# Kernel tuning notes

Hardware: AMD Instinct MI355X
Metric: run time of the kernel (lower is better)

Reference implementation:

```python
import jax, jax.numpy as jnp
import numpy as np

B, N, K_H, K_EC = 32, 2048, 50, 5  # graphs, nodes/graph, homophily-knn k, edgeconv k


def _leaky(v):
    return jnp.where(v >= 0, v, 0.01 * v)


def _pairwise_sq(xg):
    # xg: [B,N,F] -> squared euclidean distances [B,N,N]
    s = jnp.sum(xg * xg, axis=-1)
    return s[:, :, None] + s[:, None, :] - 2.0 * jnp.einsum('bnf,bmf->bnm', xg, xg)


def _gather(xg, idx):
    # xg [B,N,F], idx [B,N,k] -> [B,N,k,F]
    return jax.vmap(lambda xs, ix: xs[ix])(xg, idx)


def _edge_conv(xg, w1, b1, w2, b2):
    # DynamicEdgeConv: knn (self included, as PyG knn), msg = nn([x_i, x_j - x_i]), aggr='add'
    d = _pairwise_sq(xg)
    _, idx = jax.lax.top_k(-d, K_EC)          # [B,N,k]
    xj = _gather(xg, idx)                      # [B,N,k,F]
    xi = jnp.broadcast_to(xg[:, :, None, :], xj.shape)
    m = jnp.concatenate([xi, xj - xi], axis=-1)
    h = _leaky(m @ w1 + b1)
    h = _leaky(h @ w2 + b2)
    return h.sum(axis=2)                       # add aggregation -> [B,N,out]


def _homophily(y, idx):
    # y [B,N], idx [B,N,k]: fraction of edges whose endpoints have equal value, per graph
    yj = jax.vmap(lambda ys, ix: ys[ix])(y, idx)
    same = (yj == y[:, :, None]).astype(jnp.float32)
    return same.mean(axis=(1, 2))              # [B]


def reference(x, pos, batch, c1w1, c1b1, c1w2, c1b2, c2w1, c2b1, c2w2, c2b2,
              l1w1, l1b1, l1w2, l1b2, mw1, mb1, mw2, mb2):
    xx = jnp.concatenate([x, pos], axis=1).reshape(B, N, 4)
    # homophily kNN graph (k=50, self-loops excluded as in knn_graph)
    d = _pairwise_sq(xx) + jnp.eye(N, dtype=xx.dtype) * 1e9
    _, hidx = jax.lax.top_k(-d, K_H)
    h = [_homophily(xx[..., c], hidx) for c in range(4)]  # hx,hy,hz,hq each [B]
    x1 = _edge_conv(xx, c1w1, c1b1, c1w2, c1b2)   # [B,N,64]
    x2 = _edge_conv(x1, c2w1, c2b1, c2w2, c2b2)   # shared conv2 weights
    x3 = _edge_conv(x2, c2w1, c2b1, c2w2, c2b2)
    feat = jnp.concatenate([xx, x1, x2, x3], axis=-1)  # [B,N,196]
    o = _leaky(feat @ l1w1 + l1b1) @ l1w2 + l1b2       # lin1 -> [B,N,256]
    o = o.mean(axis=1)                                  # global_mean_pool -> [B,256]
    o = jnp.concatenate([o] + [hh[:, None] for hh in h], axis=1)  # [B,260]
    o = _leaky(o)
    o = _leaky(o @ mw1 + mb1)
    return o @ mw2 + mb2                                # [B,cla]


def setup_inputs() -> dict:
    key = jax.random.key(0)
    ks = jax.random.split(key, 20)

    def lin(k, fin, fout):
        kw, kb = jax.random.split(k)
        s = 1.0 / np.sqrt(fin)
        return (jax.random.uniform(kw, (fin, fout), jnp.float32, -s, s),
                jax.random.uniform(kb, (fout,), jnp.float32, -s, s))

    x = jax.random.normal(ks[0], (B * N, 1), jnp.float32)
    pos = jax.random.normal(ks[1], (B * N, 3), jnp.float32)
    batch = jnp.repeat(jnp.arange(B, dtype=jnp.int64), N)
    c1w1, c1b1 = lin(ks[2], 8, 64)
    c1w2, c1b2 = lin(ks[3], 64, 64)
    c2w1, c2b1 = lin(ks[4], 128, 128)
    c2w2, c2b2 = lin(ks[5], 128, 64)
    l1w1, l1b1 = lin(ks[6], 196, 512)
    l1w2, l1b2 = lin(ks[7], 512, 256)
    mw1, mb1 = lin(ks[8], 260, 256)
    mw2, mb2 = lin(ks[9], 256, 3)
    return dict(x=x, pos=pos, batch=batch,
                c1w1=c1w1, c1b1=c1b1, c1w2=c1w2, c1b2=c1b2,
                c2w1=c2w1, c2b1=c2b1, c2w2=c2w2, c2b2=c2b2,
                l1w1=l1w1, l1b1=l1b1, l1w2=l1w2, l1b2=l1b2,
                mw1=mw1, mb1=mb1, mw2=mw2, mb2=mb2)
```

## Files before the change

### kernel.cpp

```cpp
#include <hip/hip_runtime.h>

static constexpr int B = 32, N = 2048, BN = B * N;

#define DEV static __device__ __forceinline__

typedef _Float16 half_t;
typedef __attribute__((ext_vector_type(8))) _Float16 half8;
typedef __attribute__((ext_vector_type(4))) _Float16 half4;
typedef __attribute__((ext_vector_type(4))) float f32x4;
typedef unsigned long long u64;

DEV float lk(float v) { return v >= 0.f ? v : 0.01f * v; }
DEV bool lexlt(float d1, int j1, float d2, int j2) {
    return d1 < d2 || (d1 == d2 && j1 < j2);
}

DEV unsigned int mono(float f) {
    unsigned int b = __float_as_uint(f);
    return b ^ ((unsigned int)((int)b >> 31) | 0x80000000u);
}
DEV float unmono(unsigned int v) {
    unsigned int b = (v & 0x80000000u) ? (v & 0x7fffffffu) : ~v;
    return __uint_as_float(b);
}
DEV u64 pk(float d, int j) {
    return ((u64)mono(d) << 32) | (unsigned int)j;
}
static constexpr u64 KINIT = 0xFF800000ull << 32 | 0x7fffffffull;

DEV int mbcnt64(unsigned long long m) {
    return __builtin_amdgcn_mbcnt_hi((unsigned)(m >> 32),
                                     __builtin_amdgcn_mbcnt_lo((unsigned)m, 0));
}
DEV float dist4s(float4 a, float sa, float4 b, float sb) {
    float dt = fmaf(a.x, b.x, fmaf(a.y, b.y, fmaf(a.z, b.z, a.w * b.w)));
    return (sa + sb) - 2.f * dt;
}

__global__ __launch_bounds__(256) void k_build_xx(const float* __restrict__ x,
                                                  const float* __restrict__ pos,
                                                  float* __restrict__ xx,
                                                  float* __restrict__ sq) {
    int i = blockIdx.x * 256 + threadIdx.x;
    if (i < BN) {
        float4 v;
        v.x = x[i];
        v.y = pos[3 * i + 0];
        v.z = pos[3 * i + 1];
        v.w = pos[3 * i + 2];
        ((float4*)xx)[i] = v;
        sq[i] = fmaf(v.x, v.x, fmaf(v.y, v.y, fmaf(v.z, v.z, v.w * v.w)));
    }
}

__global__ __launch_bounds__(256, 8) void k_knn4(const float* __restrict__ xx,
                                                 const float* __restrict__ sq,
                                                 int* __restrict__ c1idx,
                                                 unsigned int* __restrict__ hpart) {
    int gw = (blockIdx.x * 256 + threadIdx.x) >> 6;
    int lane = threadIdx.x & 63;
    int g = gw >> 11, i = gw & 2047;
    int lane_self = i & 63, t_self = i >> 6;
    const float4* base = ((const float4*)xx) + g * N;
    const float* sqb = sq + g * N;
    float4 xi = base[i];
    float si = sqb[i];

    unsigned int u[32];
    unsigned int L[6];
    unsigned int eqany = 0;
#pragma unroll
    for (int s = 0; s < 6; s++) L[s] = 0xFFFFFFFFu;
#pragma unroll 4
    for (int t = 0; t < 32; t++) {
        float4 xj = base[lane + 64 * t];
        float sj = sqb[lane + 64 * t];
        unsigned int nv = mono(dist4s(xi, si, xj, sj));
        u[t] = nv;
        bool eq = (xj.x == xi.x) | (xj.y == xi.y) | (xj.z == xi.z) | (xj.w == xi.w);
        bool notself = (lane + 64 * t) != i;
        eqany |= (eq && notself) ? (1u << t) : 0u;
#pragma unroll
        for (int s = 0; s < 6; s++) {
            unsigned int lo_ = min(L[s], nv);
            nv = max(L[s], nv);
            L[s] = lo_;
        }
    }
    unsigned int uself = 0x80000000u;
    bool haveEq = (__ballot(eqany != 0) != 0ULL);

    unsigned int lo = L[0], hi = L[0];
#pragma unroll
    for (int o = 1; o < 64; o <<= 1) {
        lo = min(lo, (unsigned int)__shfl_xor((int)lo, o));
        hi = max(hi, (unsigned int)__shfl_xor((int)hi, o));
    }
    unsigned int cp = lo ^ hi;
    int msb = cp ? (31 - __builtin_clz(cp)) : -1;
    unsigned int prefix = (msb >= 0) ? (hi & ~((2u << msb) - 1u)) : lo;

    unsigned int vA = prefix, vB = prefix;
    if (haveEq) {
#pragma unroll 1
        for (int bit = msb; bit >= 0; --bit) {
            unsigned int cA = vA | (1u << bit);
            unsigned int cB = vB | (1u << bit);
            int cntA = 0, cntB = 0;
#pragma unroll
            for (int s = 0; s < 6; s++) cntA += (int)__popcll(__ballot(L[s] < cA));
#pragma unroll
            for (int s = 0; s < 5; s++) cntB += (int)__popcll(__ballot(L[s] < cB));
            cntA -= (uself < cA) ? 1 : 0;
            if (cntA < 50) vA = cA;
            if (cntB < 5) vB = cB;
        }
        if (__ballot(L[5] < vA) != 0ULL) {
            vA = prefix;
#pragma unroll 1
            for (int bit = msb; bit >= 0; --bit) {
                unsigned int c = vA | (1u << bit);
                int cnt = 0;
#pragma unroll
                for (int t = 0; t < 32; t++) cnt += (int)__popcll(__ballot(u[t] < c));
                cnt -= (uself < c) ? 1 : 0;
                if (cnt < 50) vA = c;
            }
        }
    } else {
#pragma unroll 1
        for (int bit = msb; bit >= 0; --bit) {
            unsigned int cB = vB | (1u << bit);
            int cntB = 0;
#pragma unroll
            for (int s = 0; s < 5; s++) cntB += (int)__popcll(__ballot(L[s] < cB));
            if (cntB < 5) vB = cB;
        }
    }

    unsigned int rawB = 0, eqBm = 0;
#pragma unroll
    for (int t = 0; t < 32; t++) {
        rawB |= (u[t] < vB ? 1u : 0u) << t;
        eqBm |= (u[t] == vB ? 1u : 0u) << t;
    }
    unsigned int packB = (unsigned)__popc(rawB) | ((unsigned)__popc(eqBm) << 16);

    if (haveEq) {
        unsigned int rawA = 0, eqAm = 0;
#pragma unroll
        for (int t = 0; t < 32; t++) {
            rawA |= (u[t] < vA ? 1u : 0u) << t;
            eqAm |= (u[t] == vA ? 1u : 0u) << t;
        }
        unsigned int packA = (unsigned)__popc(rawA) | ((unsigned)__popc(eqAm) << 16);
#pragma unroll
        for (int o = 1; o < 64; o <<= 1) packA += __shfl_xor(packA, o);
        int cltA = (int)(packA & 0xffffu) - ((uself < vA) ? 1 : 0);
        int ceqA = (int)(packA >> 16) - ((uself == vA) ? 1 : 0);

        int neededA = 50 - cltA;
        bool allEqA = (ceqA == neededA);
        unsigned int selAm = rawA, eqAs = eqAm;
        if (lane == lane_self) {
            selAm &= ~(1u << t_self);
            eqAs &= ~(1u << t_self);
        }
        unsigned int hm = allEqA ? (selAm | eqAs) : selAm;
        int c0 = 0, c1 = 0, c2 = 0, c3 = 0;
        unsigned int mm = hm;
        while (mm) {
            int t = __ffs(mm) - 1;
            mm &= mm - 1;
            float4 xj = base[lane + 64 * t];
            c0 += (xj.x == xi.x) ? 1 : 0;
            c1 += (xj.y == xi.y) ? 1 : 0;
            c2 += (xj.z == xi.z) ? 1 : 0;
            c3 += (xj.w == xi.w) ? 1 : 0;
        }
        if (!allEqA) {
            unsigned int em = eqAs;
            for (int r = 0; r < neededA; r++) {
                int mt = __ffs(em) - 1;
                int mj = (mt >= 0) ? (lane + 64 * mt) : 0x7fffffff;
                int bm = mj;
#pragma unroll
                for (int o = 1; o < 64; o <<= 1) bm = min(bm, __shfl_xor(bm, o));
                if (mj == bm && mt >= 0) {
                    em &= ~(1u << mt);
                    float4 xj = base[lane + 64 * mt];
                    c0 += (xj.x == xi.x) ? 1 : 0;
                    c1 += (xj.y == xi.y) ? 1 : 0;
                    c2 += (xj.z == xi.z) ? 1 : 0;
                    c3 += (xj.w == xi.w) ? 1 : 0;
                }
            }
        }
        unsigned int pc = (unsigned)c0 | ((unsigned)c1 << 8) | ((unsigned)c2 << 16) | ((unsigned)c3 << 24);
#pragma unroll
        for (int o = 1; o < 64; o <<= 1) pc += __shfl_xor(pc, o);
        if (lane == 0) hpart[gw] = pc;
    } else {
        if (lane == 0) hpart[gw] = 0u;
    }

#pragma unroll
    for (int o = 1; o < 64; o <<= 1) packB += __shfl_xor(packB, o);
    int cltB = (int)(packB & 0xffffu);
    int ceqB = (int)(packB >> 16);
    int neededB = 5 - cltB;
    bool allEqB = (ceqB == neededB);
    unsigned int selBm = allEqB ? (rawB | eqBm) : rawB;
    int base_slot = 0;
#pragma unroll 4
    for (int t = 0; t < 32; t++) {
        bool take = (selBm >> t) & 1;
        unsigned long long m = __ballot(take);
        if (take) c1idx[gw * 5 + base_slot + mbcnt64(m)] = lane + 64 * t;
        base_slot += (int)__popcll(m);
    }
    if (!allEqB) {
        unsigned int em = eqBm;
        for (int r = 0; r < neededB; r++) {
            int mt = __ffs(em) - 1;
            int mj = (mt >= 0) ? (lane + 64 * mt) : 0x7fffffff;
            int bm = mj;
#pragma unroll
            for (int o = 1; o < 64; o <<= 1) bm = min(bm, __shfl_xor(bm, o));
            if (mj == bm && mt >= 0) {
                em &= ~(1u << mt);
                c1idx[gw * 5 + base_slot + r] = bm;
            }
        }
    }
}

__global__ __launch_bounds__(256) void k_split(const float* __restrict__ X,
                                               half_t* __restrict__ Xh,
                                               half_t* __restrict__ Xl,
                                               float* __restrict__ s) {
    int row = (blockIdx.x * 256 + threadIdx.x) >> 6;
    int lane = threadIdx.x & 63;
    float x = X[(size_t)row * 64 + lane];
    half_t h = (half_t)x;
    half_t l = (half_t)(x - (float)h);
    Xh[(size_t)row * 64 + lane] = h;
    Xl[(size_t)row * 64 + lane] = l;
    float ss = x * x;
#pragma unroll
    for (int o = 1; o < 64; o <<= 1) ss += __shfl_xor(ss, o);
    if (lane == 0) s[row] = ss;
}

template <int F, int C>
__global__ __launch_bounds__(256, 4) void k_pq(const float* __restrict__ X,
                                               const float* __restrict__ w1,
                                               const float* __restrict__ b1,
                                               float* __restrict__ p,
                                               float* __restrict__ q) {
    constexpr int FS = F + 4;
    __shared__ __align__(16) float Xs[64 * FS];
    __shared__ __align__(16) float Ws[64 * FS];
    int nbase = blockIdx.x * 64;
    int cchunk = blockIdx.y;
    int tx = threadIdx.x & 15, ty = threadIdx.x >> 4;
    for (int idx = threadIdx.x; idx < 64 * (F / 4); idx += 256) {
        int r = idx / (F / 4), fq = idx % (F / 4);
        float4 v = ((const float4*)(X + (size_t)(nbase + r) * F))[fq];
        *(float4*)&Xs[r * FS + fq * 4] = v;
    }
    for (int idx = threadIdx.x; idx < 64 * F; idx += 256) {
        int f = idx >> 6, cl = idx & 63;
        int ccg = cchunk * 64 + cl;
        float v;
        if (ccg < C) v = w1[f * C + ccg] - w1[(F + f) * C + ccg];
        else         v = w1[(F + f) * C + (ccg - C)];
        Ws[cl * FS + f] = v;
    }
    __syncthreads();
    float acc[4][4];
#pragma unroll
    for (int a = 0; a < 4; a++)
#pragma unroll
        for (int b = 0; b < 4; b++) acc[a][b] = 0.f;
#pragma unroll 2
    for (int fs = 0; fs < F / 4; fs++) {
        float4 xv[4], wv[4];
#pragma unroll
        for (int a = 0; a < 4; a++) xv[a] = *(const float4*)&Xs[(ty + 16 * a) * FS + fs * 4];
#pragma unroll
        for (int b = 0; b < 4; b++) wv[b] = *(const float4*)&Ws[(tx + 16 * b) * FS + fs * 4];
#pragma unroll
        for (int a = 0; a < 4; a++)
#pragma unroll
            for (int b = 0; b < 4; b++) {
                acc[a][b] = fmaf(xv[a].x, wv[b].x, acc[a][b]);
                acc[a][b] = fmaf(xv[a].y, wv[b].y, acc[a][b]);
                acc[a][b] = fmaf(xv[a].z, wv[b].z, acc[a][b]);
                acc[a][b] = fmaf(xv[a].w, wv[b].w, acc[a][b]);
            }
    }
#pragma unroll
    for (int a = 0; a < 4; a++) {
        int n = nbase + ty + 16 * a;
#pragma unroll
        for (int b = 0; b < 4; b++) {
            int ccg = cchunk * 64 + tx + 16 * b;
            if (ccg < C) p[(size_t)n * C + ccg] = acc[a][b] + b1[ccg];
            else         q[(size_t)n * C + (ccg - C)] = acc[a][b];
        }
    }
}

template <int C1>
__global__ __launch_bounds__(256, 4) void k_edge(const float* __restrict__ p,
                                                 const float* __restrict__ q,
                                                 const int* __restrict__ cidx,
                                                 const float* __restrict__ w2,
                                                 const float* __restrict__ b2,
                                                 float* __restrict__ Xout) {
    __shared__ __align__(16) float h1[80 * 68];
    __shared__ __align__(16) float w2T[64 * 68];
    int nb = blockIdx.x * 16;
    int gb = (nb >> 11) << 11;
    int tx = threadIdx.x & 15, ty = threadIdx.x >> 4;
    float acc[5][4];
#pragma unroll
    for (int m = 0; m < 5; m++)
#pragma unroll
        for (int n = 0; n < 4; n++) acc[m][n] = 0.f;
#pragma unroll 1
    for (int half = 0; half < C1 / 64; half++) {
        __syncthreads();
        for (int idx = threadIdx.x; idx < 64 * 64; idx += 256) {
            int l = idx >> 6, c = idx & 63;
            w2T[c * 68 + l] = w2[(half * 64 + l) * 64 + c];
        }
        for (int idx = threadIdx.x; idx < 80 * 16; idx += 256) {
            int e = idx >> 4, fq = idx & 15;
            int node = nb + e / 5, kk = e - 5 * (e / 5);
            int j = cidx[node * 5 + kk];
            float4 pv = ((const float4*)(p + (size_t)node * C1 + half * 64))[fq];
            float4 qv = ((const float4*)(q + (size_t)(gb + j) * C1 + half * 64))[fq];
            float4 hv;
            hv.x = lk(pv.x + qv.x); hv.y = lk(pv.y + qv.y);
            hv.z = lk(pv.z + qv.z); hv.w = lk(pv.w + qv.w);
            *(float4*)&h1[e * 68 + fq * 4] = hv;
        }
        __syncthreads();
#pragma unroll 1
        for (int ls = 0; ls < 16; ls++) {
            float4 hv[5], wf[4];
#pragma unroll
            for (int m = 0; m < 5; m++) hv[m] = *(const float4*)&h1[(ty + 16 * m) * 68 + ls * 4];
#pragma unroll
            for (int n = 0; n < 4; n++) wf[n] = *(const float4*)&w2T[(tx + 16 * n) * 68 + ls * 4];
#pragma unroll
            for (int m = 0; m < 5; m++)
#pragma unroll
                for (int n = 0; n < 4; n++) {
                    acc[m][n] = fmaf(hv[m].x, wf[n].x, acc[m][n]);
                    acc[m][n] = fmaf(hv[m].y, wf[n].y, acc[m][n]);
                    acc[m][n] = fmaf(hv[m].z, wf[n].z, acc[m][n]);
                    acc[m][n] = fmaf(hv[m].w, wf[n].w, acc[m][n]);
                }
        }
    }
    float b2r[4];
#pragma unroll
    for (int n = 0; n < 4; n++) b2r[n] = b2[tx + 16 * n];
    __syncthreads();
    float* h2 = h1;
#pragma unroll
    for (int m = 0; m < 5; m++)
#pragma unroll
        for (int n = 0; n < 4; n++)
            h2[(ty + 16 * m) * 68 + (tx + 16 * n)] = lk(acc[m][n] + b2r[n]);
    __syncthreads();
#pragma unroll
    for (int rr = 0; rr < 4; rr++) {
        int idx = threadIdx.x + 256 * rr;
        int node = idx >> 6, c = idx & 63;
        float sum = 0.f;
#pragma unroll
        for (int kk = 0; kk < 5; kk++) sum += h2[(node * 5 + kk) * 68 + c];
        Xout[(size_t)(nb + node) * 64 + c] = sum;
    }
}

__global__ __launch_bounds__(256) void k_knn64(const half_t* __restrict__ Xh,
                                               const half_t* __restrict__ Xl,
                                               const float* __restrict__ s,
                                               float2* __restrict__ cand) {
    __shared__ __align__(16) char smem[20480];
    int g = blockIdx.x, it = blockIdx.y, bz = blockIdx.z;
    int gbase = g * 2048, ibase = it * 64;
    int lane = threadIdx.x & 63, wave = threadIdx.x >> 6;
    int m = lane & 15, quad = lane >> 4;

    const half_t* ahp = Xh + (size_t)(gbase + ibase + wave * 16 + m) * 64 + quad * 8;
    const half_t* alp = Xl + (size_t)(gbase + ibase + wave * 16 + m) * 64 + quad * 8;
    half8 Ah0 = *(const half8*)(ahp);
    half8 Ah1 = *(const half8*)(ahp + 32);
    half8 Al0 = *(const half8*)(alp);
    half8 Al1 = *(const half8*)(alp + 32);
    float si_r[4];
#pragma unroll
    for (int reg = 0; reg < 4; reg++)
        si_r[reg] = s[gbase + ibase + wave * 16 + quad * 4 + reg];

    u64 K[4][5];
    float thv[4];
#pragma unroll
    for (int a = 0; a < 4; a++) {
        thv[a] = __builtin_inff();
#pragma unroll
        for (int ss = 0; ss < 5; ss++) K[a][ss] = KINIT;
    }

    int jt0 = bz * 8;
    const half_t* pbh = Xh + (size_t)(gbase + jt0 * 64 + m) * 64 + quad * 8;
    const half_t* pbl = Xl + (size_t)(gbase + jt0 * 64 + m) * 64 + quad * 8;
    const float* psn = s + gbase + jt0 * 64 + m;
    int jvc = jt0 * 64 + m;

    half8 Pbh0[2], Pbh1[2], Pbl0[2], Pbl1[2];
    float Psj[2];
    Pbh0[0] = *(const half8*)(pbh);
    Pbh1[0] = *(const half8*)(pbh + 32);
    Pbl0[0] = *(const half8*)(pbl);
    Pbl1[0] = *(const half8*)(pbl + 32);
    Psj[0] = *psn;
    pbh += 1024; pbl += 1024; psn += 16;

#pragma unroll 1
    for (int jtl = 0; jtl < 8; jtl++) {
#pragma unroll
        for (int reg = 0; reg < 4; reg++) {
            float th = unmono((unsigned int)(K[reg][4] >> 32));
            th = fminf(th, __shfl_xor(th, 1));
            th = fminf(th, __shfl_xor(th, 2));
            th = fminf(th, __shfl_xor(th, 4));
            th = fminf(th, __shfl_xor(th, 8));
            thv[reg] = th;
        }
#pragma unroll
        for (int sub = 0; sub < 4; sub++) {
            int cur = sub & 1, nxt = cur ^ 1;
            if (sub < 3 || jtl < 7) {
                Pbh0[nxt] = *(const half8*)(pbh);
                Pbh1[nxt] = *(const half8*)(pbh + 32);
                Pbl0[nxt] = *(const half8*)(pbl);
                Pbl1[nxt] = *(const half8*)(pbl + 32);
                Psj[nxt] = *psn;
                pbh += 1024; pbl += 1024; psn += 16;
            }
            f32x4 ahh = {0.f, 0.f, 0.f, 0.f};
            f32x4 ahl = {0.f, 0.f, 0.f, 0.f};
            f32x4 alh = {0.f, 0.f, 0.f, 0.f};
            f32x4 all = {0.f, 0.f, 0.f, 0.f};
            ahh = __builtin_amdgcn_mfma_f32_16x16x32_f16(Ah0, Pbh0[cur], ahh, 0, 0, 0);
            ahl = __builtin_amdgcn_mfma_f32_16x16x32_f16(Ah0, Pbl0[cur], ahl, 0, 0, 0);
            alh = __builtin_amdgcn_mfma_f32_16x16x32_f16(Al0, Pbh0[cur], alh, 0, 0, 0);
            all = __builtin_amdgcn_mfma_f32_16x16x32_f16(Al0, Pbl0[cur], all, 0, 0, 0);
            ahh = __builtin_amdgcn_mfma_f32_16x16x32_f16(Ah1, Pbh1[cur], ahh, 0, 0, 0);
            ahl = __builtin_amdgcn_mfma_f32_16x16x32_f16(Ah1, Pbl1[cur], ahl, 0, 0, 0);
            alh = __builtin_amdgcn_mfma_f32_16x16x32_f16(Al1, Pbh1[cur], alh, 0, 0, 0);
            all = __builtin_amdgcn_mfma_f32_16x16x32_f16(Al1, Pbl1[cur], all, 0, 0, 0);
            float sjv = Psj[cur];
            int jv = jvc;
            jvc += 16;
#pragma unroll
            for (int reg = 0; reg < 4; reg++) {
                float dot = ((all[reg] + alh[reg]) + ahl[reg]) + ahh[reg];
                float dv = (si_r[reg] + sjv) - 2.f * dot;
                if (__any(dv <= thv[reg])) {
                    if (dv <= thv[reg]) {
                        u64 nk = pk(dv, jv);
                        if (nk < K[reg][4]) {
                            K[reg][4] = nk;
#pragma unroll
                            for (int ss = 4; ss >= 1; ss--)
                                if (K[reg][ss] < K[reg][ss - 1]) {
                                    u64 t = K[reg][ss]; K[reg][ss] = K[reg][ss - 1]; K[reg][ss - 1] = t;
                                }
                        }
                    }
                }
            }
        }
    }

#pragma unroll
    for (int reg = 0; reg < 4; reg++) {
        u64 pv[5];
#pragma unroll
        for (int ss = 0; ss < 5; ss++) pv[ss] = __shfl_xor(K[reg][ss], 1);
        if ((lane & 1) == 0) {
#pragma unroll
            for (int c = 0; c < 5; c++) {
                if (pv[c] < K[reg][4]) {
                    K[reg][4] = pv[c];
#pragma unroll
                    for (int ss = 4; ss >= 1; ss--)
                        if (K[reg][ss] < K[reg][ss - 1]) {
                            u64 t = K[reg][ss]; K[reg][ss] = K[reg][ss - 1]; K[reg][ss - 1] = t;
                        }
                }
            }
        }
    }

    u64* candk = (u64*)smem;
    int rowbase = wave * 16 + quad * 4;
    if ((lane & 1) == 0) {
#pragma unroll
        for (int reg = 0; reg < 4; reg++)
#pragma unroll
            for (int ss = 0; ss < 5; ss++)
                candk[(rowbase + reg) * 40 + (m >> 1) * 5 + ss] = K[reg][ss];
    }
    __syncthreads();
    if (threadIdx.x < 64) {
        int row = threadIdx.x;
        u64 fk[5];
#pragma unroll
        for (int ss = 0; ss < 5; ss++) fk[ss] = KINIT;
#pragma unroll 1
        for (int c = 0; c < 40; c++) {
            u64 k = candk[row * 40 + c];
            if (k < fk[4]) {
                fk[4] = k;
#pragma unroll
                for (int ss = 4; ss >= 1; ss--)
                    if (fk[ss] < fk[ss - 1]) {
                        u64 t = fk[ss]; fk[ss] = fk[ss - 1]; fk[ss - 1] = t;
                    }
            }
        }
#pragma unroll
        for (int ss = 0; ss < 5; ss++) {
            float2 e;
            e.x = unmono((unsigned int)(fk[ss] >> 32));
            e.y = __int_as_float((int)(unsigned int)(fk[ss] & 0xffffffffu));
            cand[((size_t)(gbase + ibase + row) * 4 + bz) * 5 + ss] = e;
        }
    }
}

__global__ __launch_bounds__(256) void k_knn_merge(const float2* __restrict__ cand,
                                                   int* __restrict__ cidx) {
    int row = blockIdx.x * 256 + threadIdx.x;
    if (row >= BN) return;
    float fv[5];
    int fj[5];
#pragma unroll
    for (int ss = 0; ss < 5; ss++) { fv[ss] = __builtin_inff(); fj[ss] = 0x7fffffff; }
#pragma unroll
    for (int c = 0; c < 20; c++) {
        float2 e = cand[(size_t)row * 20 + c];
        float dv = e.x;
        int jv = __float_as_int(e.y);
        if (lexlt(dv, jv, fv[4], fj[4])) {
            fv[4] = dv; fj[4] = jv;
#pragma unroll
            for (int ss = 4; ss >= 1; ss--)
                if (lexlt(fv[ss], fj[ss], fv[ss - 1], fj[ss - 1])) {
                    float tv = fv[ss]; fv[ss] = fv[ss - 1]; fv[ss - 1] = tv;
                    int tj = fj[ss]; fj[ss] = fj[ss - 1]; fj[ss - 1] = tj;
                }
        }
    }
#pragma unroll
    for (int ss = 0; ss < 5; ss++) cidx[(size_t)row * 5 + ss] = fj[ss];
}

__global__ __launch_bounds__(256) void k_wsplit(const float* __restrict__ w1,
                                                half_t* __restrict__ WhT,
                                                half_t* __restrict__ WlT) {
    int idx = blockIdx.x * 256 + threadIdx.x;
    if (idx >= 512 * 224) return;
    int c = idx / 224, f = idx - c * 224;
    float v = (f < 196) ? w1[(size_t)f * 512 + c] : 0.f;
    half_t h = (half_t)v;
    WhT[(size_t)c * 224 + f] = h;
    WlT[(size_t)c * 224 + f] = (half_t)(v - (float)h);
}

__global__ __launch_bounds__(256) void k_fsplit(const float* __restrict__ xx,
                                                const float* __restrict__ x1,
                                                const float* __restrict__ x2,
                                                const float* __restrict__ x3,
                                                half_t* __restrict__ Fh,
                                                half_t* __restrict__ Fl) {
    int nb = blockIdx.x * 64;
    for (int idx = threadIdx.x; idx < 64 * 56; idx += 256) {
        int r = idx / 56, sg = idx - r * 56;
        int node = nb + r;
        float4 v;
        if (sg == 0)       v = ((const float4*)xx)[node];
        else if (sg < 17)  v = ((const float4*)(x1 + (size_t)node * 64))[sg - 1];
        else if (sg < 33)  v = ((const float4*)(x2 + (size_t)node * 64))[sg - 17];
        else if (sg < 49)  v = ((const float4*)(x3 + (size_t)node * 64))[sg - 33];
        else { v.x = 0.f; v.y = 0.f; v.z = 0.f; v.w = 0.f; }
        float f0 = v.x, f1 = v.y, f2 = v.z, f3 = v.w;
        half_t h0 = (half_t)f0, h1 = (half_t)f1, h2 = (half_t)f2, h3 = (half_t)f3;
        half4 hv = {h0, h1, h2, h3};
        half4 lv = {(half_t)(f0 - (float)h0), (half_t)(f1 - (float)h1),
                    (half_t)(f2 - (float)h2), (half_t)(f3 - (float)h3)};
        *(half4*)(Fh + (size_t)node * 224 + sg * 4) = hv;
        *(half4*)(Fl + (size_t)node * 224 + sg * 4) = lv;
    }
}

__global__ __launch_bounds__(256) void k_lin1m(const half_t* __restrict__ Fh,
                                               const half_t* __restrict__ Fl,
                                               const half_t* __restrict__ WhT,
                                               const half_t* __restrict__ WlT,
                                               const float* __restrict__ b1,
                                               float* __restrict__ Hpart) {
    __shared__ __align__(16) half_t Bh[16 * 232];
    __shared__ __align__(16) half_t Bl[16 * 232];
    __shared__ float pool[4][512];
    int zb = blockIdx.x, g = blockIdx.y;
    int lane = threadIdx.x & 63, wave = threadIdx.x >> 6;
    int m = lane & 15, quad = lane >> 4;
    for (int i = threadIdx.x; i < 4 * 512; i += 256) ((float*)pool)[i] = 0.f;
    int node = g * 2048 + zb * 64 + wave * 16 + m;
    const half_t* fh = Fh + (size_t)node * 224 + quad * 8;
    const half_t* fl = Fl + (size_t)node * 224 + quad * 8;
    half8 Ah[7], Al[7];
#pragma unroll
    for (int ks = 0; ks < 7; ks++) {
        Ah[ks] = *(const half8*)(fh + ks * 32);
        Al[ks] = *(const half8*)(fl + ks * 32);
    }
    __syncthreads();
#pragma unroll 1
    for (int ct = 0; ct < 32; ct++) {
        for (int idx = threadIdx.x; idx < 448; idx += 256) {
            int r = idx / 28, cc = idx - r * 28;
            *(half8*)&Bh[r * 232 + cc * 8] = *(const half8*)(WhT + (size_t)(ct * 16 + r) * 224 + cc * 8);
            *(half8*)&Bl[r * 232 + cc * 8] = *(const half8*)(WlT + (size_t)(ct * 16 + r) * 224 + cc * 8);
        }
        __syncthreads();
        f32x4 a1 = {0.f, 0.f, 0.f, 0.f};
        f32x4 a2 = {0.f, 0.f, 0.f, 0.f};
#pragma unroll
        for (int ks = 0; ks < 7; ks++) {
            half8 bh = *(const half8*)&Bh[m * 232 + ks * 32 + quad * 8];
            half8 bl = *(const half8*)&Bl[m * 232 + ks * 32 + quad * 8];
            a1 = __builtin_amdgcn_mfma_f32_16x16x32_f16(Ah[ks], bh, a1, 0, 0, 0);
            a2 = __builtin_amdgcn_mfma_f32_16x16x32_f16(Ah[ks], bl, a2, 0, 0, 0);
            a2 = __builtin_amdgcn_mfma_f32_16x16x32_f16(Al[ks], bh, a2, 0, 0, 0);
        }
        float bb = b1[ct * 16 + m];
        float sacc = 0.f;
#pragma unroll
        for (int reg = 0; reg < 4; reg++) sacc += lk((a1[reg] + a2[reg]) + bb);
        sacc += __shfl_xor(sacc, 16);
        sacc += __shfl_xor(sacc, 32);
        if (quad == 0) pool[wave][ct * 16 + m] += sacc;
        __syncthreads();
    }
    for (int c = threadIdx.x; c < 512; c += 256) {
        float v = pool[0][c] + pool[1][c] + pool[2][c] + pool[3][c];
        Hpart[((size_t)zb * 32 + g) * 512 + c] = v;
    }
}

__global__ __launch_bounds__(256) void k_final(const float* __restrict__ Hpart,
                                               const unsigned int* __restrict__ hpart,
                                               const float* __restrict__ l1w2,
                                               const float* __restrict__ l1b2,
                                               const float* __restrict__ mw1,
                                               const float* __restrict__ mb1,
                                               const float* __restrict__ mw2,
                                               const float* __restrict__ mb2,
                                               float* __restrict__ out) {
    __shared__ float Hb[512];
    __shared__ float z[260];
    __shared__ float y[256];
    __shared__ unsigned int hsum[4];
    int g = blockIdx.x, t = threadIdx.x;
    if (t < 4) hsum[t] = 0;
    __syncthreads();
    unsigned int s0 = 0, s1 = 0, s2 = 0, s3 = 0;
#pragma unroll
    for (int r = 0; r < 8; r++) {
        unsigned int v = hpart[g * 2048 + t + 256 * r];
        s0 += v & 0xffu; s1 += (v >> 8) & 0xffu;
        s2 += (v >> 16) & 0xffu; s3 += (v >> 24) & 0xffu;
    }
    atomicAdd(&hsum[0], s0); atomicAdd(&hsum[1], s1);
    atomicAdd(&hsum[2], s2); atomicAdd(&hsum[3], s3);
#pragma unroll
    for (int half = 0; half < 2; half++) {
        int c = t + 256 * half;
        float v = 0.f;
#pragma unroll
        for (int zz = 0; zz < 32; zz++) v += Hpart[((size_t)zz * 32 + g) * 512 + c];
        Hb[c] = v * (1.f / 2048.f);
    }
    __syncthreads();
    float acc = l1b2[t];
    for (int f = 0; f < 512; f++) acc = fmaf(Hb[f], l1w2[f * 256 + t], acc);
    z[t] = lk(acc);
    if (t < 4) z[256 + t] = lk((float)hsum[t] * (1.f / (2048.f * 50.f)));
    __syncthreads();
    float acc2 = mb1[t];
    for (int f = 0; f < 260; f++) acc2 = fmaf(z[f], mw1[f * 256 + t], acc2);
    y[t] = lk(acc2);
    __syncthreads();
    if (t < 3) {
        float a = mb2[t];
        for (int c = 0; c < 256; c++) a = fmaf(y[c], mw2[c * 3 + t], a);
        out[g * 3 + t] = a;
    }
}

extern "C" void kernel_launch(void* const* d_in, const int* in_sizes, int n_in,
                              void* d_out, int out_size, void* d_ws, size_t ws_size,
                              hipStream_t stream) {
    (void)in_sizes; (void)n_in; (void)out_size; (void)ws_size;
    const float* x    = (const float*)d_in[0];
    const float* pos  = (const float*)d_in[1];
    const float* c1w1 = (const float*)d_in[3];
    const float* c1b1 = (const float*)d_in[4];
    const float* c1w2 = (const float*)d_in[5];
    const float* c1b2 = (const float*)d_in[6];
    const float* c2w1 = (const float*)d_in[7];
    const float* c2b1 = (const float*)d_in[8];
    const float* c2w2 = (const float*)d_in[9];
    const float* c2b2 = (const float*)d_in[10];
    const float* l1w1 = (const float*)d_in[11];
    const float* l1b1 = (const float*)d_in[12];
    const float* l1w2 = (const float*)d_in[13];
    const float* l1b2 = (const float*)d_in[14];
    const float* mw1  = (const float*)d_in[15];
    const float* mb1  = (const float*)d_in[16];
    const float* mw2  = (const float*)d_in[17];
    const float* mb2  = (const float*)d_in[18];
    float* out = (float*)d_out;

    char* w = (char*)d_ws;
    auto alloc = [&](size_t bytes) -> void* {
        void* r = (void*)w;
        w += (bytes + 255) & ~(size_t)255;
        return r;
    };
    float* xx   = (float*)alloc((size_t)BN * 4 * 4);
    float* pbuf = (float*)alloc((size_t)BN * 128 * 4);
    float* qbuf = (float*)alloc((size_t)BN * 128 * 4);
    float* x1   = (float*)alloc((size_t)BN * 64 * 4);
    float* x2   = (float*)alloc((size_t)BN * 64 * 4);
    float* x3   = (float*)alloc((size_t)BN * 64 * 4);
    float* sbuf = (float*)alloc((size_t)BN * 4);
    float* sq4  = (float*)alloc((size_t)BN * 4);
    half_t* xh  = (half_t*)alloc((size_t)BN * 64 * 2);
    half_t* xl  = (half_t*)alloc((size_t)BN * 64 * 2);
    int* c1i    = (int*)alloc((size_t)BN * 5 * 4);
    int* c2i    = (int*)alloc((size_t)BN * 5 * 4);
    int* c3i    = (int*)alloc((size_t)BN * 5 * 4);
    unsigned int* hpart = (unsigned int*)alloc((size_t)BN * 4);
    float* Hpart = (float*)alloc((size_t)32 * 32 * 512 * 4);
    float2* cand = (float2*)alloc((size_t)BN * 20 * 8);
    half_t* Fh  = (half_t*)alloc((size_t)BN * 224 * 2);
    half_t* Fl  = (half_t*)alloc((size_t)BN * 224 * 2);
    half_t* WhT = (half_t*)alloc((size_t)512 * 224 * 2);
    half_t* WlT = (half_t*)alloc((size_t)512 * 224 * 2);

    k_build_xx<<<BN / 256, 256, 0, stream>>>(x, pos, xx, sq4);
    k_wsplit<<<(512 * 224 + 255) / 256, 256, 0, stream>>>(l1w1, WhT, WlT);
    k_knn4<<<BN / 4, 256, 0, stream>>>(xx, sq4, c1i, hpart);
    k_pq<4, 64><<<dim3(BN / 64, 2), 256, 0, stream>>>(xx, c1w1, c1b1, pbuf, qbuf);
    k_edge<64><<<BN / 16, 256, 0, stream>>>(pbuf, qbuf, c1i, c1w2, c1b2, x1);
    k_split<<<BN / 4, 256, 0, stream>>>(x1, xh, xl, sbuf);
    k_knn64<<<dim3(32, 32, 4), 256, 0, stream>>>(xh, xl, sbuf, cand);
    k_knn_merge<<<BN / 256, 256, 0, stream>>>(cand, c2i);
    k_pq<64, 128><<<dim3(BN / 64, 4), 256, 0, stream>>>(x1, c2w1, c2b1, pbuf, qbuf);
    k_edge<128><<<BN / 16, 256, 0, stream>>>(pbuf, qbuf, c2i, c2w2, c2b2, x2);
    k_split<<<BN / 4, 256, 0, stream>>>(x2, xh, xl, sbuf);
    k_knn64<<<dim3(32, 32, 4), 256, 0, stream>>>(xh, xl, sbuf, cand);
    k_knn_merge<<<BN / 256, 256, 0, stream>>>(cand, c3i);
    k_pq<64, 128><<<dim3(BN / 64, 4), 256, 0, stream>>>(x2, c2w1, c2b1, pbuf, qbuf);
    k_edge<128><<<BN / 16, 256, 0, stream>>>(pbuf, qbuf, c3i, c2w2, c2b2, x3);
    k_fsplit<<<BN / 64, 256, 0, stream>>>(xx, x1, x2, x3, Fh, Fl);
    k_lin1m<<<dim3(32, 32), 256, 0, stream>>>(Fh, Fl, WhT, WlT, l1b1, Hpart);
    k_final<<<32, 256, 0, stream>>>(Hpart, hpart, l1w2, l1b2, mw1, mb1, mw2, mb2, out);
}
```

Baseline: 1.360 ms.

## Fuse kNN merge and fp16 split into edge-conv kernel, pair ballot checks

The kNN candidate merge now runs at the start of k_edge, with 16 threads per block writing the selected neighbours to shared memory. The fp16 hi/lo split and row-norm computation now run in the k_edge epilogue. This removes four kernel launches and the round trips of x and the index buffers through global memory. Separately, the knn64 inner loop computes all four distances first and issues one __any ballot per pair of rows instead of one per row. The cost is a serial 20-candidate merge done by 16 threads while the other threads wait at the barrier.

```diff
diff --git a/kernel.cpp b/kernel.cpp
--- a/kernel.cpp
+++ b/kernel.cpp
@@ -233,23 +233,6 @@
             }
         }
     }
-}
-
-__global__ __launch_bounds__(256) void k_split(const float* __restrict__ X,
-                                               half_t* __restrict__ Xh,
-                                               half_t* __restrict__ Xl,
-                                               float* __restrict__ s) {
-    int row = (blockIdx.x * 256 + threadIdx.x) >> 6;
-    int lane = threadIdx.x & 63;
-    float x = X[(size_t)row * 64 + lane];
-    half_t h = (half_t)x;
-    half_t l = (half_t)(x - (float)h);
-    Xh[(size_t)row * 64 + lane] = h;
-    Xl[(size_t)row * 64 + lane] = l;
-    float ss = x * x;
-#pragma unroll
-    for (int o = 1; o < 64; o <<= 1) ss += __shfl_xor(ss, o);
-    if (lane == 0) s[row] = ss;
 }
 
 template <int F, int C>
@@ -312,18 +295,51 @@
     }
 }
 
-template <int C1>
+template <int C1, bool MERGE, bool SPLIT>
 __global__ __launch_bounds__(256, 4) void k_edge(const float* __restrict__ p,
                                                  const float* __restrict__ q,
                                                  const int* __restrict__ cidx,
+                                                 const float2* __restrict__ cand,
                                                  const float* __restrict__ w2,
                                                  const float* __restrict__ b2,
-                                                 float* __restrict__ Xout) {
+                                                 float* __restrict__ Xout,
+                                                 half_t* __restrict__ Xh,
+                                                 half_t* __restrict__ Xl,
+                                                 float* __restrict__ srow) {
     __shared__ __align__(16) float h1[80 * 68];
     __shared__ __align__(16) float w2T[64 * 68];
+    __shared__ int cidx5[16 * 5];
     int nb = blockIdx.x * 16;
     int gb = (nb >> 11) << 11;
     int tx = threadIdx.x & 15, ty = threadIdx.x >> 4;
+
+    if (MERGE) {
+        if (threadIdx.x < 16) {
+            int node = nb + threadIdx.x;
+            float fv[5];
+            int fj[5];
+#pragma unroll
+            for (int ss = 0; ss < 5; ss++) { fv[ss] = __builtin_inff(); fj[ss] = 0x7fffffff; }
+#pragma unroll 1
+            for (int c = 0; c < 20; c++) {
+                float2 e = cand[(size_t)node * 20 + c];
+                float dv = e.x;
+                int jv = __float_as_int(e.y);
+                if (lexlt(dv, jv, fv[4], fj[4])) {
+                    fv[4] = dv; fj[4] = jv;
+#pragma unroll
+                    for (int ss = 4; ss >= 1; ss--)
+                        if (lexlt(fv[ss], fj[ss], fv[ss - 1], fj[ss - 1])) {
+                            float tv = fv[ss]; fv[ss] = fv[ss - 1]; fv[ss - 1] = tv;
+                            int tj = fj[ss]; fj[ss] = fj[ss - 1]; fj[ss - 1] = tj;
+                        }
+                }
+            }
+#pragma unroll
+            for (int ss = 0; ss < 5; ss++) cidx5[threadIdx.x * 5 + ss] = fj[ss];
+        }
+    }
+
     float acc[5][4];
 #pragma unroll
     for (int m = 0; m < 5; m++)
@@ -338,8 +354,9 @@
         }
         for (int idx = threadIdx.x; idx < 80 * 16; idx += 256) {
             int e = idx >> 4, fq = idx & 15;
-            int node = nb + e / 5, kk = e - 5 * (e / 5);
-            int j = cidx[node * 5 + kk];
+            int nloc = e / 5, kk = e - 5 * nloc;
+            int node = nb + nloc;
+            int j = MERGE ? cidx5[nloc * 5 + kk] : cidx[node * 5 + kk];
             float4 pv = ((const float4*)(p + (size_t)node * C1 + half * 64))[fq];
             float4 qv = ((const float4*)(q + (size_t)(gb + j) * C1 + half * 64))[fq];
             float4 hv;
@@ -384,7 +401,18 @@
         float sum = 0.f;
 #pragma unroll
         for (int kk = 0; kk < 5; kk++) sum += h2[(node * 5 + kk) * 68 + c];
-        Xout[(size_t)(nb + node) * 64 + c] = sum;
+        int gnode = nb + node;
+        Xout[(size_t)gnode * 64 + c] = sum;
+        if (SPLIT) {
+            half_t h = (half_t)sum;
+            half_t l = (half_t)(sum - (float)h);
+            Xh[(size_t)gnode * 64 + c] = h;
+            Xl[(size_t)gnode * 64 + c] = l;
+            float ss2 = sum * sum;
+#pragma unroll
+            for (int o = 1; o < 64; o <<= 1) ss2 += __shfl_xor(ss2, o);
+            if (c == 0) srow[gnode] = ss2;
+        }
     }
 }
 
@@ -470,19 +498,37 @@
             float sjv = Psj[cur];
             int jv = jvc;
             jvc += 16;
+            float dvr[4];
 #pragma unroll
             for (int reg = 0; reg < 4; reg++) {
                 float dot = ((all[reg] + alh[reg]) + ahl[reg]) + ahh[reg];
-                float dv = (si_r[reg] + sjv) - 2.f * dot;
-                if (__any(dv <= thv[reg])) {
-                    if (dv <= thv[reg]) {
-                        u64 nk = pk(dv, jv);
-                        if (nk < K[reg][4]) {
-                            K[reg][4] = nk;
+                dvr[reg] = (si_r[reg] + sjv) - 2.f * dot;
+            }
+#pragma unroll
+            for (int pr = 0; pr < 2; pr++) {
+                int r0 = 2 * pr, r1 = 2 * pr + 1;
+                bool c0 = (dvr[r0] <= thv[r0]);
+                bool c1 = (dvr[r1] <= thv[r1]);
+                if (__any(c0 || c1)) {
+                    if (c0) {
+                        u64 nk = pk(dvr[r0], jv);
+                        if (nk < K[r0][4]) {
+                            K[r0][4] = nk;
 #pragma unroll
                             for (int ss = 4; ss >= 1; ss--)
-                                if (K[reg][ss] < K[reg][ss - 1]) {
-                                    u64 t = K[reg][ss]; K[reg][ss] = K[reg][ss - 1]; K[reg][ss - 1] = t;
+                                if (K[r0][ss] < K[r0][ss - 1]) {
+                                    u64 t = K[r0][ss]; K[r0][ss] = K[r0][ss - 1]; K[r0][ss - 1] = t;
+                                }
+                        }
+                    }
+                    if (c1) {
+                        u64 nk = pk(dvr[r1], jv);
+                        if (nk < K[r1][4]) {
+                            K[r1][4] = nk;
+#pragma unroll
+                            for (int ss = 4; ss >= 1; ss--)
+                                if (K[r1][ss] < K[r1][ss - 1]) {
+                                    u64 t = K[r1][ss]; K[r1][ss] = K[r1][ss - 1]; K[r1][ss - 1] = t;
                                 }
                         }
                     }
@@ -546,33 +592,6 @@
             cand[((size_t)(gbase + ibase + row) * 4 + bz) * 5 + ss] = e;
         }
     }
-}
-
-__global__ __launch_bounds__(256) void k_knn_merge(const float2* __restrict__ cand,
-                                                   int* __restrict__ cidx) {
-    int row = blockIdx.x * 256 + threadIdx.x;
-    if (row >= BN) return;
-    float fv[5];
-    int fj[5];
-#pragma unroll
-    for (int ss = 0; ss < 5; ss++) { fv[ss] = __builtin_inff(); fj[ss] = 0x7fffffff; }
-#pragma unroll
-    for (int c = 0; c < 20; c++) {
-        float2 e = cand[(size_t)row * 20 + c];
-        float dv = e.x;
-        int jv = __float_as_int(e.y);
-        if (lexlt(dv, jv, fv[4], fj[4])) {
-            fv[4] = dv; fj[4] = jv;
-#pragma unroll
-            for (int ss = 4; ss >= 1; ss--)
-                if (lexlt(fv[ss], fj[ss], fv[ss - 1], fj[ss - 1])) {
-                    float tv = fv[ss]; fv[ss] = fv[ss - 1]; fv[ss - 1] = tv;
-                    int tj = fj[ss]; fj[ss] = fj[ss - 1]; fj[ss - 1] = tj;
-                }
-        }
-    }
-#pragma unroll
-    for (int ss = 0; ss < 5; ss++) cidx[(size_t)row * 5 + ss] = fj[ss];
 }
 
 __global__ __launch_bounds__(256) void k_wsplit(const float* __restrict__ w1,
@@ -760,8 +779,6 @@
     half_t* xh  = (half_t*)alloc((size_t)BN * 64 * 2);
     half_t* xl  = (half_t*)alloc((size_t)BN * 64 * 2);
     int* c1i    = (int*)alloc((size_t)BN * 5 * 4);
-    int* c2i    = (int*)alloc((size_t)BN * 5 * 4);
-    int* c3i    = (int*)alloc((size_t)BN * 5 * 4);
     unsigned int* hpart = (unsigned int*)alloc((size_t)BN * 4);
     float* Hpart = (float*)alloc((size_t)32 * 32 * 512 * 4);
     float2* cand = (float2*)alloc((size_t)BN * 20 * 8);
@@ -774,17 +791,16 @@
     k_wsplit<<<(512 * 224 + 255) / 256, 256, 0, stream>>>(l1w1, WhT, WlT);
     k_knn4<<<BN / 4, 256, 0, stream>>>(xx, sq4, c1i, hpart);
     k_pq<4, 64><<<dim3(BN / 64, 2), 256, 0, stream>>>(xx, c1w1, c1b1, pbuf, qbuf);
-    k_edge<64><<<BN / 16, 256, 0, stream>>>(pbuf, qbuf, c1i, c1w2, c1b2, x1);
-    k_split<<<BN / 4, 256, 0, stream>>>(x1, xh, xl, sbuf);
+    k_edge<64, false, true><<<BN / 16, 256, 0, stream>>>(pbuf, qbuf, c1i, nullptr,
+                                                         c1w2, c1b2, x1, xh, xl, sbuf);
     k_knn64<<<dim3(32, 32, 4), 256, 0, stream>>>(xh, xl, sbuf, cand);
-    k_knn_merge<<<BN / 256, 256, 0, stream>>>(cand, c2i);
     k_pq<64, 128><<<dim3(BN / 64, 4), 256, 0, stream>>>(x1, c2w1, c2b1, pbuf, qbuf);
-    k_edge<128><<<BN / 16, 256, 0, stream>>>(pbuf, qbuf, c2i, c2w2, c2b2, x2);
-    k_split<<<BN / 4, 256, 0, stream>>>(x2, xh, xl, sbuf);
+    k_edge<128, true, true><<<BN / 16, 256, 0, stream>>>(pbuf, qbuf, nullptr, cand,
+                                                         c2w2, c2b2, x2, xh, xl, sbuf);
     k_knn64<<<dim3(32, 32, 4), 256, 0, stream>>>(xh, xl, sbuf, cand);
-    k_knn_merge<<<BN / 256, 256, 0, stream>>>(cand, c3i);
     k_pq<64, 128><<<dim3(BN / 64, 4), 256, 0, stream>>>(x2, c2w1, c2b1, pbuf, qbuf);
-    k_edge<128><<<BN / 16, 256, 0, stream>>>(pbuf, qbuf, c3i, c2w2, c2b2, x3);
+    k_edge<128, true, false><<<BN / 16, 256, 0, stream>>>(pbuf, qbuf, nullptr, cand,
+                                                          c2w2, c2b2, x3, nullptr, nullptr, nullptr);
     k_fsplit<<<BN / 64, 256, 0, stream>>>(xx, x1, x2, x3, Fh, Fl);
     k_lin1m<<<dim3(32, 32), 256, 0, stream>>>(Fh, Fl, WhT, WlT, l1b1, Hpart);
     k_final<<<32, 256, 0, stream>>>(Hpart, hpart, l1w2, l1b2, mw1, mb1, mw2, mb2, out);
```

Result: no change. 1.373 ms (+1.0%).
